# Kernel tuning notes

Hardware: AMD Instinct MI355X
Metric: run time of the kernel (lower is better)

Reference implementation:

```python
import jax, jax.numpy as jnp
import numpy as np

H = 1024        # pegasus-large hidden size
HEADS = 16      # matches the hard-coded /16 in the source
T = 512         # decoder steps
N = 1024        # encoder (source) tokens
V = 96103       # pegasus tokenizer vocab size


def setup_inputs() -> dict:
    key = jax.random.key(0)
    ks = jax.random.split(key, 8)
    return {
        "cross_attn": jax.random.normal(ks[0], (1, HEADS, T, N), jnp.float32),
        "encoder_hidden": jax.random.normal(ks[1], (1, N, H), jnp.float32),
        "decoder_hidden": jax.random.normal(ks[2], (1, T, H), jnp.float32),
        "decoder_embedding": jax.random.normal(ks[3], (1, T, H), jnp.float32),
        "logits": jax.random.normal(ks[4], (1, T, V), jnp.float32),
        "input_ids": jax.random.randint(ks[5], (N,), 0, V),
        "pointer_w": jax.random.normal(ks[6], (1, 3 * H), jnp.float32) * 0.02,
        "pointer_b": jnp.zeros((1,), jnp.float32),
    }


def reference(cross_attn, encoder_hidden, decoder_hidden, decoder_embedding,
              logits, input_ids, pointer_w, pointer_b):
    # squeeze batch dim (module assumes batch=1)
    ca = jnp.sum(cross_attn[0], axis=0) / 16.0                 # [T, N] head-avg cross attn
    enc = encoder_hidden[0]                                    # [N, H]
    dec_h = decoder_hidden[0]                                  # [T, H]
    dec_e = decoder_embedding[0]                               # [T, H]
    lg = logits[0]                                             # [T, V]

    h = ca @ enc                                               # [T, H] attn-weighted context
    lin = jnp.concatenate([h, dec_h, dec_e], axis=1)           # [T, 3H]
    gen_probs = jax.nn.sigmoid(lin @ pointer_w.T + pointer_b)  # [T, 1]

    distribution = jax.nn.softmax(lg, axis=1)                  # [T, V]
    gen_logits = gen_probs * distribution                      # [T, V]

    # vectorized form of: for t, for n: copy_logits[t, input_ids[n]] = ca[t, n]
    Tn, Vn = lg.shape
    rows = jnp.broadcast_to(jnp.arange(Tn)[:, None], ca.shape)       # [T, N]
    cols = jnp.broadcast_to(input_ids[None, :], ca.shape)            # [T, N]
    copy_logits = jnp.zeros((Tn, Vn), lg.dtype).at[rows, cols].set(ca)

    final_probs = gen_logits + (1.0 - gen_probs) * copy_logits  # [T, V]
    return gen_probs, final_probs
```

## Files before the change

### kernel.cpp

```cpp
#include <hip/hip_runtime.h>

#define Tn 512
#define Nn 1024
#define Hn 1024
#define Vn 96103
#define NHEADS 16
#define SPLITS 16
#define CHUNK 6007

typedef float f4 __attribute__((ext_vector_type(4)));

__global__ __launch_bounds__(256) void k_headsum(const float* __restrict__ attn,
                                                 float* __restrict__ ca,
                                                 int* __restrict__ col2n) {
  int i = blockIdx.x * 256 + threadIdx.x;
  if (i < Vn) col2n[i] = -1;
  const f4* a4 = (const f4*)attn;
  const int slice = (Tn * Nn) / 4;
  f4 acc = __builtin_nontemporal_load(&a4[i]);
#pragma unroll
  for (int h = 1; h < NHEADS; ++h) {
    f4 v = __builtin_nontemporal_load(&a4[h * slice + i]);
    acc += v;
  }
  ((f4*)ca)[i] = acc * (1.0f / 16.0f);
}

__global__ __launch_bounds__(256) void k_ew(const float* __restrict__ enc,
                                            const float* __restrict__ w,
                                            float* __restrict__ ew,
                                            const int* __restrict__ ids,
                                            int* __restrict__ col2n) {
  int n = blockIdx.x, tid = threadIdx.x;
  if (tid == 0) atomicMax(&col2n[ids[n]], n);
  float4 r = ((const float4*)(enc + n * Hn))[tid];
  float4 ww = ((const float4*)w)[tid];
  float p = r.x * ww.x + r.y * ww.y + r.z * ww.z + r.w * ww.w;
  for (int off = 32; off > 0; off >>= 1) p += __shfl_down(p, off, 64);
  __shared__ float lds[4];
  int lane = tid & 63, wv = tid >> 6;
  if (lane == 0) lds[wv] = p;
  __syncthreads();
  if (tid == 0) ew[n] = lds[0] + lds[1] + lds[2] + lds[3];
}

__global__ __launch_bounds__(256) void k_gen(const float* __restrict__ ca,
                                             const float* __restrict__ ew,
                                             const float* __restrict__ dh,
                                             const float* __restrict__ de,
                                             const float* __restrict__ w,
                                             const float* __restrict__ b,
                                             float* __restrict__ gen,
                                             float* __restrict__ out_gen) {
  int t = blockIdx.x, tid = threadIdx.x;
  float4 c4 = ((const float4*)(ca + t * Nn))[tid];
  float4 e4 = ((const float4*)ew)[tid];
  float p = c4.x * e4.x + c4.y * e4.y + c4.z * e4.z + c4.w * e4.w;
  float4 h4 = ((const float4*)(dh + t * Hn))[tid];
  float4 w1 = ((const float4*)(w + Hn))[tid];
  p += h4.x * w1.x + h4.y * w1.y + h4.z * w1.z + h4.w * w1.w;
  float4 d4 = ((const float4*)(de + t * Hn))[tid];
  float4 w2 = ((const float4*)(w + 2 * Hn))[tid];
  p += d4.x * w2.x + d4.y * w2.y + d4.z * w2.z + d4.w * w2.w;
  for (int off = 32; off > 0; off >>= 1) p += __shfl_down(p, off, 64);
  __shared__ float lds[4];
  int lane = tid & 63, wv = tid >> 6;
  if (lane == 0) lds[wv] = p;
  __syncthreads();
  if (tid == 0) {
    float z = lds[0] + lds[1] + lds[2] + lds[3] + b[0];
    float g = 1.0f / (1.0f + __expf(-z));
    gen[t] = g;
    out_gen[t] = g;
  }
}

__global__ __launch_bounds__(256) void k_statpart(const float* __restrict__ lg,
                                                  float* __restrict__ part_m,
                                                  float* __restrict__ part_s) {
  const int c = blockIdx.x, t = blockIdx.y;
  const int tid = threadIdx.x;
  const unsigned vbeg = c * CHUNK;
  const unsigned vend = min(vbeg + CHUNK, (unsigned)Vn);
  const unsigned beg = (unsigned)t * Vn + vbeg;
  const unsigned end = (unsigned)t * Vn + vend;
  const unsigned beg4 = (beg + 3u) & ~3u;
  const unsigned end4 = end & ~3u;

  float m = -INFINITY, s = 0.0f;
  for (unsigned i = beg + tid; i < beg4; i += 256) {
    float x = lg[i];
    if (x > m) { s *= __expf(m - x); m = x; }
    s += __expf(x - m);
  }
  const float4* lg4 = (const float4*)lg;
  for (unsigned i4 = beg4 / 4 + tid; i4 < end4 / 4; i4 += 256) {
    float4 a = lg4[i4];
    float mx = fmaxf(fmaxf(a.x, a.y), fmaxf(a.z, a.w));
    if (mx > m) { s *= __expf(m - mx); m = mx; }
    s += __expf(a.x - m) + __expf(a.y - m) + __expf(a.z - m) + __expf(a.w - m);
  }
  for (unsigned i = end4 + tid; i < end; i += 256) {
    float x = lg[i];
    if (x > m) { s *= __expf(m - x); m = x; }
    s += __expf(x - m);
  }
  for (int off = 32; off > 0; off >>= 1) {
    float mo = __shfl_down(m, off, 64);
    float so = __shfl_down(s, off, 64);
    float M = fmaxf(m, mo);
    s = s * __expf(m - M) + so * __expf(mo - M);
    m = M;
  }
  __shared__ float lm[4], ls[4];
  int lane = tid & 63, wv = tid >> 6;
  if (lane == 0) { lm[wv] = m; ls[wv] = s; }
  __syncthreads();
  if (tid == 0) {
    float M = fmaxf(fmaxf(lm[0], lm[1]), fmaxf(lm[2], lm[3]));
    float S = ls[0] * __expf(lm[0] - M) + ls[1] * __expf(lm[1] - M) +
              ls[2] * __expf(lm[2] - M) + ls[3] * __expf(lm[3] - M);
    part_m[t * SPLITS + c] = M;
    part_s[t * SPLITS + c] = S;
  }
}

__global__ __launch_bounds__(256) void k_statcombine(const float* __restrict__ part_m,
                                                     const float* __restrict__ part_s,
                                                     const float* __restrict__ gen,
                                                     float4* __restrict__ params) {
  int t = blockIdx.x * 256 + threadIdx.x;
  if (t >= Tn) return;
  float M = -INFINITY, S = 0.0f;
#pragma unroll
  for (int c = 0; c < SPLITS; ++c) {
    float mp = part_m[t * SPLITS + c];
    float sp = part_s[t * SPLITS + c];
    float Mn = fmaxf(M, mp);
    S = S * __expf(M - Mn) + sp * __expf(mp - Mn);
    M = Mn;
  }
  float g = gen[t];
  params[t] = make_float4(g, M, 1.0f / S, 1.0f - g);
}

__global__ __launch_bounds__(256) void k_final(const float* __restrict__ lg,
                                               const float* __restrict__ ca,
                                               const float4* __restrict__ params,
                                               const int* __restrict__ col2n,
                                               float* __restrict__ out) {
  const unsigned total4 = ((unsigned)Tn * (unsigned)Vn) / 4u;
  const f4* lg4 = (const f4*)lg;
  f4* out4 = (f4*)out;
  for (unsigned i4 = blockIdx.x * 256u + threadIdx.x; i4 < total4;
       i4 += gridDim.x * 256u) {
    unsigned i0 = i4 * 4u;
    unsigned t = i0 / (unsigned)Vn;
    unsigned v = i0 - t * (unsigned)Vn;
    f4 x = __builtin_nontemporal_load(&lg4[i4]);
    f4 r;
    if (v + 3u < (unsigned)Vn) {
      float4 P = params[t];
      int n0 = col2n[v], n1 = col2n[v + 1], n2 = col2n[v + 2], n3 = col2n[v + 3];
      r[0] = P.x * __expf(x[0] - P.y) * P.z;
      r[1] = P.x * __expf(x[1] - P.y) * P.z;
      r[2] = P.x * __expf(x[2] - P.y) * P.z;
      r[3] = P.x * __expf(x[3] - P.y) * P.z;
      const float* cat = ca + t * Nn;
      if (n0 >= 0) r[0] += P.w * cat[n0];
      if (n1 >= 0) r[1] += P.w * cat[n1];
      if (n2 >= 0) r[2] += P.w * cat[n2];
      if (n3 >= 0) r[3] += P.w * cat[n3];
    } else {
#pragma unroll
      for (int j = 0; j < 4; ++j) {
        unsigned idx = i0 + j;
        unsigned tt = idx / (unsigned)Vn;
        unsigned vv = idx - tt * (unsigned)Vn;
        float4 P = params[tt];
        int n = col2n[vv];
        float val = P.x * __expf(x[j] - P.y) * P.z;
        if (n >= 0) val += P.w * ca[tt * Nn + n];
        r[j] = val;
      }
    }
    __builtin_nontemporal_store(r, &out4[i4]);
  }
}

extern "C" void kernel_launch(void* const* d_in, const int* in_sizes, int n_in,
                              void* d_out, int out_size, void* d_ws, size_t ws_size,
                              hipStream_t stream) {
  const float* attn = (const float*)d_in[0];
  const float* enc  = (const float*)d_in[1];
  const float* dh   = (const float*)d_in[2];
  const float* de   = (const float*)d_in[3];
  const float* lg   = (const float*)d_in[4];
  const int*   ids  = (const int*)d_in[5];
  const float* w    = (const float*)d_in[6];
  const float* b    = (const float*)d_in[7];
  float* out = (float*)d_out;

  float4* params = (float4*)d_ws;
  float* ca     = (float*)(params + Tn);
  float* ew     = ca + Tn * Nn;
  float* gen    = ew + Nn;
  float* part_m = gen + Tn;
  float* part_s = part_m + Tn * SPLITS;
  int*   col2n  = (int*)(part_s + Tn * SPLITS);

  hipLaunchKernelGGL(k_headsum, dim3((Tn * Nn / 4) / 256), dim3(256), 0, stream,
                     attn, ca, col2n);
  hipLaunchKernelGGL(k_ew, dim3(Nn), dim3(256), 0, stream, enc, w, ew, ids, col2n);
  hipLaunchKernelGGL(k_gen, dim3(Tn), dim3(256), 0, stream, ca, ew, dh, de, w, b, gen, out);
  hipLaunchKernelGGL(k_statpart, dim3(SPLITS, Tn), dim3(256), 0, stream, lg, part_m, part_s);
  hipLaunchKernelGGL(k_statcombine, dim3((Tn + 255) / 256), dim3(256), 0, stream,
                     part_m, part_s, gen, params);
  hipLaunchKernelGGL(k_final, dim3(4096), dim3(256), 0, stream,
                     lg, ca, params, col2n, out + Tn);
}
```

Measured before the change: 124.8 us.

## Merge six launches into three by fusing independent stages into block-partitioned kernels

Measured after the change: 117.9 us. 1.06x faster.

```diff
diff --git a/kernel.cpp b/kernel.cpp
--- a/kernel.cpp
+++ b/kernel.cpp
@@ -8,51 +8,118 @@
 #define SPLITS 16
 #define CHUNK 6007
 
+#define HS_BLKS 512
+#define EW_BLKS 1024
+#define SP_BLKS (SPLITS*Tn)
+#define K0_BLKS (HS_BLKS + EW_BLKS + SP_BLKS)
+
 typedef float f4 __attribute__((ext_vector_type(4)));
 
-__global__ __launch_bounds__(256) void k_headsum(const float* __restrict__ attn,
-                                                 float* __restrict__ ca,
-                                                 int* __restrict__ col2n) {
-  int i = blockIdx.x * 256 + threadIdx.x;
-  if (i < Vn) col2n[i] = -1;
-  const f4* a4 = (const f4*)attn;
-  const int slice = (Tn * Nn) / 4;
-  f4 acc = __builtin_nontemporal_load(&a4[i]);
+__global__ __launch_bounds__(256) void k0(const float* __restrict__ attn,
+                                          const float* __restrict__ enc,
+                                          const float* __restrict__ w,
+                                          const float* __restrict__ lg,
+                                          float* __restrict__ ca,
+                                          float* __restrict__ ew,
+                                          float* __restrict__ part_m,
+                                          float* __restrict__ part_s,
+                                          int* __restrict__ col2n) {
+  const int b = blockIdx.x, tid = threadIdx.x;
+
+  if (b < HS_BLKS) {
+    int i = b * 256 + tid;
+    if (i < Vn) col2n[i] = -1;
+    const f4* a4 = (const f4*)attn;
+    const int slice = (Tn * Nn) / 4;
+    f4 acc = __builtin_nontemporal_load(&a4[i]);
 #pragma unroll
-  for (int h = 1; h < NHEADS; ++h) {
-    f4 v = __builtin_nontemporal_load(&a4[h * slice + i]);
-    acc += v;
-  }
-  ((f4*)ca)[i] = acc * (1.0f / 16.0f);
-}
-
-__global__ __launch_bounds__(256) void k_ew(const float* __restrict__ enc,
-                                            const float* __restrict__ w,
-                                            float* __restrict__ ew,
-                                            const int* __restrict__ ids,
-                                            int* __restrict__ col2n) {
-  int n = blockIdx.x, tid = threadIdx.x;
-  if (tid == 0) atomicMax(&col2n[ids[n]], n);
-  float4 r = ((const float4*)(enc + n * Hn))[tid];
-  float4 ww = ((const float4*)w)[tid];
-  float p = r.x * ww.x + r.y * ww.y + r.z * ww.z + r.w * ww.w;
-  for (int off = 32; off > 0; off >>= 1) p += __shfl_down(p, off, 64);
-  __shared__ float lds[4];
-  int lane = tid & 63, wv = tid >> 6;
-  if (lane == 0) lds[wv] = p;
-  __syncthreads();
-  if (tid == 0) ew[n] = lds[0] + lds[1] + lds[2] + lds[3];
-}
-
-__global__ __launch_bounds__(256) void k_gen(const float* __restrict__ ca,
-                                             const float* __restrict__ ew,
-                                             const float* __restrict__ dh,
-                                             const float* __restrict__ de,
-                                             const float* __restrict__ w,
-                                             const float* __restrict__ b,
-                                             float* __restrict__ gen,
-                                             float* __restrict__ out_gen) {
-  int t = blockIdx.x, tid = threadIdx.x;
+    for (int h = 1; h < NHEADS; ++h)
+      acc += __builtin_nontemporal_load(&a4[h * slice + i]);
+    ((f4*)ca)[i] = acc * (1.0f / 16.0f);
+    return;
+  }
+
+  if (b < HS_BLKS + EW_BLKS) {
+    int n = b - HS_BLKS;
+    float4 r = ((const float4*)(enc + n * Hn))[tid];
+    float4 ww = ((const float4*)w)[tid];
+    float p = r.x * ww.x + r.y * ww.y + r.z * ww.z + r.w * ww.w;
+    for (int off = 32; off > 0; off >>= 1) p += __shfl_down(p, off, 64);
+    __shared__ float lds[4];
+    int lane = tid & 63, wv = tid >> 6;
+    if (lane == 0) lds[wv] = p;
+    __syncthreads();
+    if (tid == 0) ew[n] = lds[0] + lds[1] + lds[2] + lds[3];
+    return;
+  }
+
+  {
+    int rem = b - HS_BLKS - EW_BLKS;
+    const int c = rem & (SPLITS - 1), t = rem >> 4;
+    const unsigned vbeg = c * CHUNK;
+    const unsigned vend = min(vbeg + CHUNK, (unsigned)Vn);
+    const unsigned beg = (unsigned)t * Vn + vbeg;
+    const unsigned end = (unsigned)t * Vn + vend;
+    const unsigned beg4 = (beg + 3u) & ~3u;
+    const unsigned end4 = end & ~3u;
+
+    float m = -INFINITY, s = 0.0f;
+    for (unsigned i = beg + tid; i < beg4; i += 256) {
+      float x = lg[i];
+      if (x > m) { s *= __expf(m - x); m = x; }
+      s += __expf(x - m);
+    }
+    const float4* lg4 = (const float4*)lg;
+    for (unsigned i4 = beg4 / 4 + tid; i4 < end4 / 4; i4 += 256) {
+      float4 a = lg4[i4];
+      float mx = fmaxf(fmaxf(a.x, a.y), fmaxf(a.z, a.w));
+      if (mx > m) { s *= __expf(m - mx); m = mx; }
+      s += __expf(a.x - m) + __expf(a.y - m) + __expf(a.z - m) + __expf(a.w - m);
+    }
+    for (unsigned i = end4 + tid; i < end; i += 256) {
+      float x = lg[i];
+      if (x > m) { s *= __expf(m - x); m = x; }
+      s += __expf(x - m);
+    }
+    for (int off = 32; off > 0; off >>= 1) {
+      float mo = __shfl_down(m, off, 64);
+      float so = __shfl_down(s, off, 64);
+      float M = fmaxf(m, mo);
+      s = s * __expf(m - M) + so * __expf(mo - M);
+      m = M;
+    }
+    __shared__ float lm[4], ls[4];
+    int lane = tid & 63, wv = tid >> 6;
+    if (lane == 0) { lm[wv] = m; ls[wv] = s; }
+    __syncthreads();
+    if (tid == 0) {
+      float M = fmaxf(fmaxf(lm[0], lm[1]), fmaxf(lm[2], lm[3]));
+      float S = ls[0] * __expf(lm[0] - M) + ls[1] * __expf(lm[1] - M) +
+                ls[2] * __expf(lm[2] - M) + ls[3] * __expf(lm[3] - M);
+      part_m[t * SPLITS + c] = M;
+      part_s[t * SPLITS + c] = S;
+    }
+  }
+}
+
+__global__ __launch_bounds__(256) void k1(const float* __restrict__ ca,
+                                          const float* __restrict__ ew,
+                                          const float* __restrict__ dh,
+                                          const float* __restrict__ de,
+                                          const float* __restrict__ w,
+                                          const float* __restrict__ b,
+                                          const float* __restrict__ part_m,
+                                          const float* __restrict__ part_s,
+                                          const int* __restrict__ ids,
+                                          int* __restrict__ col2n,
+                                          float4* __restrict__ params,
+                                          float* __restrict__ out_gen) {
+  const int t = blockIdx.x, tid = threadIdx.x;
+  if (t == Tn) {
+    for (int n = tid; n < Nn; n += 256)
+      atomicMax(&col2n[ids[n]], n);
+    return;
+  }
   float4 c4 = ((const float4*)(ca + t * Nn))[tid];
   float4 e4 = ((const float4*)ew)[tid];
   float p = c4.x * e4.x + c4.y * e4.y + c4.z * e4.z + c4.w * e4.w;
@@ -70,85 +137,25 @@
   if (tid == 0) {
     float z = lds[0] + lds[1] + lds[2] + lds[3] + b[0];
     float g = 1.0f / (1.0f + __expf(-z));
-    gen[t] = g;
+    float M = -INFINITY, S = 0.0f;
+#pragma unroll
+    for (int c = 0; c < SPLITS; ++c) {
+      float mp = part_m[t * SPLITS + c];
+      float sp = part_s[t * SPLITS + c];
+      float Mn = fmaxf(M, mp);
+      S = S * __expf(M - Mn) + sp * __expf(mp - Mn);
+      M = Mn;
+    }
     out_gen[t] = g;
-  }
-}
-
-__global__ __launch_bounds__(256) void k_statpart(const float* __restrict__ lg,
-                                                  float* __restrict__ part_m,
-                                                  float* __restrict__ part_s) {
-  const int c = blockIdx.x, t = blockIdx.y;
-  const int tid = threadIdx.x;
-  const unsigned vbeg = c * CHUNK;
-  const unsigned vend = min(vbeg + CHUNK, (unsigned)Vn);
-  const unsigned beg = (unsigned)t * Vn + vbeg;
-  const unsigned end = (unsigned)t * Vn + vend;
-  const unsigned beg4 = (beg + 3u) & ~3u;
-  const unsigned end4 = end & ~3u;
-
-  float m = -INFINITY, s = 0.0f;
-  for (unsigned i = beg + tid; i < beg4; i += 256) {
-    float x = lg[i];
-    if (x > m) { s *= __expf(m - x); m = x; }
-    s += __expf(x - m);
-  }
-  const float4* lg4 = (const float4*)lg;
-  for (unsigned i4 = beg4 / 4 + tid; i4 < end4 / 4; i4 += 256) {
-    float4 a = lg4[i4];
-    float mx = fmaxf(fmaxf(a.x, a.y), fmaxf(a.z, a.w));
-    if (mx > m) { s *= __expf(m - mx); m = mx; }
-    s += __expf(a.x - m) + __expf(a.y - m) + __expf(a.z - m) + __expf(a.w - m);
-  }
-  for (unsigned i = end4 + tid; i < end; i += 256) {
-    float x = lg[i];
-    if (x > m) { s *= __expf(m - x); m = x; }
-    s += __expf(x - m);
-  }
-  for (int off = 32; off > 0; off >>= 1) {
-    float mo = __shfl_down(m, off, 64);
-    float so = __shfl_down(s, off, 64);
-    float M = fmaxf(m, mo);
-    s = s * __expf(m - M) + so * __expf(mo - M);
-    m = M;
-  }
-  __shared__ float lm[4], ls[4];
-  int lane = tid & 63, wv = tid >> 6;
-  if (lane == 0) { lm[wv] = m; ls[wv] = s; }
-  __syncthreads();
-  if (tid == 0) {
-    float M = fmaxf(fmaxf(lm[0], lm[1]), fmaxf(lm[2], lm[3]));
-    float S = ls[0] * __expf(lm[0] - M) + ls[1] * __expf(lm[1] - M) +
-              ls[2] * __expf(lm[2] - M) + ls[3] * __expf(lm[3] - M);
-    part_m[t * SPLITS + c] = M;
-    part_s[t * SPLITS + c] = S;
-  }
-}
-
-__global__ __launch_bounds__(256) void k_statcombine(const float* __restrict__ part_m,
-                                                     const float* __restrict__ part_s,
-                                                     const float* __restrict__ gen,
-                                                     float4* __restrict__ params) {
-  int t = blockIdx.x * 256 + threadIdx.x;
-  if (t >= Tn) return;
-  float M = -INFINITY, S = 0.0f;
-#pragma unroll
-  for (int c = 0; c < SPLITS; ++c) {
-    float mp = part_m[t * SPLITS + c];
-    float sp = part_s[t * SPLITS + c];
-    float Mn = fmaxf(M, mp);
-    S = S * __expf(M - Mn) + sp * __expf(mp - Mn);
-    M = Mn;
-  }
-  float g = gen[t];
-  params[t] = make_float4(g, M, 1.0f / S, 1.0f - g);
-}
-
-__global__ __launch_bounds__(256) void k_final(const float* __restrict__ lg,
-                                               const float* __restrict__ ca,
-                                               const float4* __restrict__ params,
-                                               const int* __restrict__ col2n,
-                                               float* __restrict__ out) {
+    params[t] = make_float4(g, M, 1.0f / S, 1.0f - g);
+  }
+}
+
+__global__ __launch_bounds__(256) void k2(const float* __restrict__ lg,
+                                          const float* __restrict__ ca,
+                                          const float4* __restrict__ params,
+                                          const int* __restrict__ col2n,
+                                          float* __restrict__ out) {
   const unsigned total4 = ((unsigned)Tn * (unsigned)Vn) / 4u;
   const f4* lg4 = (const f4*)lg;
   f4* out4 = (f4*)out;
@@ -204,18 +211,14 @@
   float4* params = (float4*)d_ws;
   float* ca     = (float*)(params + Tn);
   float* ew     = ca + Tn * Nn;
-  float* gen    = ew + Nn;
-  float* part_m = gen + Tn;
+  float* part_m = ew + Nn;
   float* part_s = part_m + Tn * SPLITS;
   int*   col2n  = (int*)(part_s + Tn * SPLITS);
 
-  hipLaunchKernelGGL(k_headsum, dim3((Tn * Nn / 4) / 256), dim3(256), 0, stream,
-                     attn, ca, col2n);
-  hipLaunchKernelGGL(k_ew, dim3(Nn), dim3(256), 0, stream, enc, w, ew, ids, col2n);
-  hipLaunchKernelGGL(k_gen, dim3(Tn), dim3(256), 0, stream, ca, ew, dh, de, w, b, gen, out);
-  hipLaunchKernelGGL(k_statpart, dim3(SPLITS, Tn), dim3(256), 0, stream, lg, part_m, part_s);
-  hipLaunchKernelGGL(k_statcombine, dim3((Tn + 255) / 256), dim3(256), 0, stream,
-                     part_m, part_s, gen, params);
-  hipLaunchKernelGGL(k_final, dim3(4096), dim3(256), 0, stream,
+  hipLaunchKernelGGL(k0, dim3(K0_BLKS), dim3(256), 0, stream,
+                     attn, enc, w, lg, ca, ew, part_m, part_s, col2n);
+  hipLaunchKernelGGL(k1, dim3(Tn + 1), dim3(256), 0, stream,
+                     ca, ew, dh, de, w, b, part_m, part_s, ids, col2n, params, out);
+  hipLaunchKernelGGL(k2, dim3(4096), dim3(256), 0, stream,
                      lg, ca, params, col2n, out + Tn);
 }
```
